# Kernel optimization log

Measured on AMD Instinct MI355X. Metric: run time of the kernel, lower is better.

## Reference

```python
import jax, jax.numpy as jnp
import numpy as np

NUM_HEADS = 4
KSIZE = 3
PAD = KSIZE // 2


def setup_inputs() -> dict:
    key = jax.random.key(0)
    ks = jax.random.split(key, 7)
    C = 128
    D = H = W = 24
    B = 1
    N = D * H * W
    std = 0.02
    return {
        "x": jax.random.normal(ks[0], (B, N, C), dtype=jnp.float32),
        "Wq": jax.random.normal(ks[1], (C, C), dtype=jnp.float32) * std,
        "bq": jnp.zeros((C,), dtype=jnp.float32),
        "Wkv": jax.random.normal(ks[2], (C, 2 * C), dtype=jnp.float32) * std,
        "bkv": jnp.zeros((2 * C,), dtype=jnp.float32),
        "Wp": jax.random.normal(ks[3], (C, C), dtype=jnp.float32) * std,
        "bp": jnp.zeros((C,), dtype=jnp.float32),
        "D": D,
        "H": H,
        "W": W,
    }


def reference(x, Wq, bq, Wkv, bkv, Wp, bp, D, H, W):
    B, N, C = x.shape
    nh = NUM_HEADS
    hc = C // nh
    scale = hc ** -0.5
    k = KSIZE
    K3 = k * k * k

    xv = x.reshape(B, D, H, W, C)
    # q: (B, D, H, W, nh, hc), pre-scaled
    q = (xv @ Wq + bq).reshape(B, D, H, W, nh, hc) * scale
    # kv: (B, D, H, W, 2, nh, hc)
    kv = (xv @ Wkv + bkv).reshape(B, D, H, W, 2, nh, hc)
    # zero-pad spatial dims (ZeroPad3d with pad_size = k//2)
    kvp = jnp.pad(kv, ((0, 0), (PAD, PAD), (PAD, PAD), (PAD, PAD), (0, 0), (0, 0), (0, 0)))
    # gather 3x3x3 neighborhoods via shifted slices (equivalent to unfold with stride=1)
    # nb: (B, D, H, W, K3, 2, nh, hc)
    nb = jnp.stack(
        [kvp[:, i:i + D, j:j + H, l:l + W]
         for i in range(k) for j in range(k) for l in range(k)],
        axis=4,
    )
    k_nb = nb[..., 0, :, :]  # (B,D,H,W,K3,nh,hc)
    v_nb = nb[..., 1, :, :]
    # per-voxel attention over K3 neighbors
    attn = jnp.einsum("bdhwnc,bdhwknc->bdhwnk", q, k_nb)
    attn = jax.nn.softmax(attn, axis=-1)
    out = jnp.einsum("bdhwnk,bdhwknc->bdhwnc", attn, v_nb)
    out = out.reshape(B, D, H, W, C) @ Wp + bp
    return out.reshape(B, N, C)
```

## Files before the change

### kernel.cpp

```cpp
#include <hip/hip_runtime.h>
#include <math.h>

#define NTOK 13824
#define CCH 128
#define DD3 24
#define SCALE 0.17677669529663687f
#define HSTRIDE 136

typedef float  f32x4  __attribute__((ext_vector_type(4)));
typedef short  s16x8  __attribute__((ext_vector_type(8)));

__device__ __forceinline__ ushort bf16_rtn(float f) {
    unsigned u = __float_as_uint(f);
    unsigned r = u + 0x7fffu + ((u >> 16) & 1u);
    return (ushort)(r >> 16);
}
__device__ __forceinline__ float bf16_f32(ushort h) {
    return __uint_as_float(((unsigned)h) << 16);
}

#define BSW(n, g) ((n) * 128 + ((((g) ^ ((n) & 7))) << 3))

__global__ __launch_bounds__(256) void prep_w(
    const float* __restrict__ Wq, const float* __restrict__ Wkv,
    const float* __restrict__ Wp, ushort* __restrict__ wimg)
{
    const int i   = blockIdx.x * 256 + threadIdx.x;
    const int seg = i >> 11;
    const int r   = i & 2047;
    const int n   = r & 63;
    const int k4  = (r >> 6) * 4;
    const float* W; int ldw, scol;
    if (seg < 2)      { W = Wq;  ldw = 128; scol = seg * 64; }
    else if (seg < 6) { W = Wkv; ldw = 256; scol = (seg - 2) * 64; }
    else              { W = Wp;  ldw = 128; scol = (seg - 6) * 64; }
    ushort4 hi, lo;
    float v;
    v = W[(k4 + 0) * ldw + scol + n]; hi.x = bf16_rtn(v); lo.x = bf16_rtn(v - bf16_f32(hi.x));
    v = W[(k4 + 1) * ldw + scol + n]; hi.y = bf16_rtn(v); lo.y = bf16_rtn(v - bf16_f32(hi.y));
    v = W[(k4 + 2) * ldw + scol + n]; hi.z = bf16_rtn(v); lo.z = bf16_rtn(v - bf16_f32(hi.z));
    v = W[(k4 + 3) * ldw + scol + n]; hi.w = bf16_rtn(v); lo.w = bf16_rtn(v - bf16_f32(hi.w));
    const int g = k4 >> 3;
    const int f = seg * 16384 + BSW(n, g) + (k4 & 7);
    *(ushort4*)(wimg + f)        = hi;
    *(ushort4*)(wimg + f + 8192) = lo;
}

__global__ __launch_bounds__(256) void qkv_fused(
    const float* __restrict__ x, const ushort* __restrict__ wimg,
    const float* __restrict__ bq, const float* __restrict__ bkv,
    float* __restrict__ qb, ushort* __restrict__ kvb)
{
    __shared__ ushort bsh[2][8192];

    const int t  = threadIdx.x;
    const int y  = blockIdx.y;
    const int wv = t >> 6, l = t & 63;

    const char* wseg = (const char*)(wimg + y * 16384);
    #pragma unroll
    for (int p = 0; p < 8; ++p) {
        const int chunk = (wv * 8 + p) * 1024;
        __builtin_amdgcn_global_load_lds(
            (const __attribute__((address_space(1))) void*)(wseg + chunk + l * 16),
            (__attribute__((address_space(3))) void*)((char*)bsh + chunk),
            16, 0, 0);
    }

    const int lm = l & 15, lk = l >> 4;
    const int row = blockIdx.x * 64 + wv * 16 + lm;
    const int ko  = lk * 8;

    s16x8 ah[4], al[4];
    #pragma unroll
    for (int kb = 0; kb < 4; ++kb) {
        const int k0 = kb * 32;
        const float4 a0 = *(const float4*)(x + row * 128 + k0 + ko);
        const float4 a1 = *(const float4*)(x + row * 128 + k0 + ko + 4);
        const float av[8] = {a0.x, a0.y, a0.z, a0.w, a1.x, a1.y, a1.z, a1.w};
        #pragma unroll
        for (int e = 0; e < 8; ++e) {
            const ushort hh = bf16_rtn(av[e]);
            ah[kb][e] = (short)hh;
            al[kb][e] = (short)bf16_rtn(av[e] - bf16_f32(hh));
        }
    }

    __syncthreads();

    f32x4 acc[4];
    #pragma unroll
    for (int nt = 0; nt < 4; ++nt)
        #pragma unroll
        for (int r = 0; r < 4; ++r) acc[nt][r] = 0.f;

    #pragma unroll
    for (int nt = 0; nt < 4; ++nt) {
        const int n = nt * 16 + lm;
        s16x8 bh[4], bl[4];
        #pragma unroll
        for (int kb = 0; kb < 4; ++kb) {
            const int g = kb * 4 + lk;
            bh[kb] = *(const s16x8*)(&bsh[0][BSW(n, g)]);
            bl[kb] = *(const s16x8*)(&bsh[1][BSW(n, g)]);
        }
        #pragma unroll
        for (int kb = 0; kb < 4; ++kb) {
            acc[nt] = __builtin_amdgcn_mfma_f32_16x16x32_bf16(ah[kb], bh[kb], acc[nt], 0, 0, 0);
            acc[nt] = __builtin_amdgcn_mfma_f32_16x16x32_bf16(ah[kb], bl[kb], acc[nt], 0, 0, 0);
            acc[nt] = __builtin_amdgcn_mfma_f32_16x16x32_bf16(al[kb], bh[kb], acc[nt], 0, 0, 0);
        }
    }

    const int orow0 = blockIdx.x * 64 + wv * 16 + lk * 4;
    #pragma unroll
    for (int nt = 0; nt < 4; ++nt) {
        const int col = y * 64 + nt * 16 + lm;
        if (col < 128) {
            const float b = bq[col];
            #pragma unroll
            for (int r = 0; r < 4; ++r)
                qb[(orow0 + r) * 128 + col] = (acc[nt][r] + b) * SCALE;
        } else {
            const int c2 = col - 128;
            const float b = bkv[c2];
            #pragma unroll
            for (int r = 0; r < 4; ++r)
                kvb[(orow0 + r) * 256 + c2] = bf16_rtn(acc[nt][r] + b);
        }
    }
}

__global__ __launch_bounds__(256) void attn3d(
    const float* __restrict__ qb, const ushort* __restrict__ kvb,
    ushort* __restrict__ aoh)
{
    __shared__ ushort sk[144 * HSTRIDE];

    const int t  = threadIdx.x;
    const int b  = blockIdx.x;
    const int tw = b % 6, th = (b / 6) % 6, td = b / 36;
    const int d0 = td * 2, h0 = th * 4, w0 = tw * 4;

    const int vox = t >> 3;
    const int q8  = t & 7;
    const int ld = vox >> 4, lh = (vox >> 2) & 3, lw = vox & 3;
    const int n  = ((d0 + ld) * DD3 + (h0 + lh)) * DD3 + (w0 + lw);
    const int choff = q8 * 16;

    float qv[16];
    #pragma unroll
    for (int m = 0; m < 4; ++m) {
        const float4 qq = *(const float4*)(qb + n * 128 + choff + m * 4);
        qv[m * 4 + 0] = qq.x; qv[m * 4 + 1] = qq.y;
        qv[m * 4 + 2] = qq.z; qv[m * 4 + 3] = qq.w;
    }

    #pragma unroll
    for (int p = 0; p < 9; ++p) {
        const int e = p * 256 + t;
        const int r = e >> 4;
        const int c = e & 15;
        const int a = r / 36, bb = (r / 6) % 6, cc = r % 6;
        const int gd = d0 - 1 + a, gh = h0 - 1 + bb, gw = w0 - 1 + cc;
        int4 v = {0, 0, 0, 0};
        if ((unsigned)gd < DD3 && (unsigned)gh < DD3 && (unsigned)gw < DD3) {
            const int n2 = (gd * DD3 + gh) * DD3 + gw;
            v = *(const int4*)(kvb + n2 * 256 + c * 8);
        }
        *(int4*)(sk + r * HSTRIDE + c * 8) = v;
    }
    __syncthreads();

    const int vbase = (ld * 36 + lh * 6 + lw);
    const ushort* kvoxel = sk + vbase * HSTRIDE + choff;

    float logit[27];
    #pragma unroll
    for (int i = 0; i < 3; ++i)
        #pragma unroll
        for (int j = 0; j < 3; ++j)
            #pragma unroll
            for (int l2 = 0; l2 < 3; ++l2) {
                const int idx = (i * 3 + j) * 3 + l2;
                const ushort* kr = kvoxel + (i * 36 + j * 6 + l2) * HSTRIDE;
                const int4 ka = *(const int4*)(kr);
                const int4 kb2 = *(const int4*)(kr + 8);
                float p = 0.f;
                const int* kwa = (const int*)&ka;
                const int* kwb = (const int*)&kb2;
                #pragma unroll
                for (int m = 0; m < 4; ++m) {
                    const unsigned u = (unsigned)kwa[m];
                    p = fmaf(qv[2 * m],     __uint_as_float(u << 16),        p);
                    p = fmaf(qv[2 * m + 1], __uint_as_float(u & 0xffff0000u), p);
                }
                #pragma unroll
                for (int m = 0; m < 4; ++m) {
                    const unsigned u = (unsigned)kwb[m];
                    p = fmaf(qv[8 + 2 * m],     __uint_as_float(u << 16),        p);
                    p = fmaf(qv[8 + 2 * m + 1], __uint_as_float(u & 0xffff0000u), p);
                }
                p += __shfl_xor(p, 1);
                logit[idx] = p;
            }

    float m0;
    {
        float t1[14];
        #pragma unroll
        for (int k = 0; k < 13; ++k) t1[k] = fmaxf(logit[2 * k], logit[2 * k + 1]);
        t1[13] = logit[26];
        float t2[7];
        #pragma unroll
        for (int k = 0; k < 7; ++k) t2[k] = fmaxf(t1[2 * k], t1[2 * k + 1]);
        m0 = fmaxf(fmaxf(fmaxf(t2[0], t2[1]), fmaxf(t2[2], t2[3])),
                   fmaxf(fmaxf(t2[4], t2[5]), t2[6]));
    }
    float s;
    {
        #pragma unroll
        for (int idx = 0; idx < 27; ++idx) logit[idx] = __expf(logit[idx] - m0);
        float t1[14];
        #pragma unroll
        for (int k = 0; k < 13; ++k) t1[k] = logit[2 * k] + logit[2 * k + 1];
        t1[13] = logit[26];
        float t2[7];
        #pragma unroll
        for (int k = 0; k < 7; ++k) t2[k] = t1[2 * k] + t1[2 * k + 1];
        s = ((t2[0] + t2[1]) + (t2[2] + t2[3])) + ((t2[4] + t2[5]) + t2[6]);
    }
    const float inv = 1.f / s;

    __syncthreads();

    #pragma unroll
    for (int p = 0; p < 9; ++p) {
        const int e = p * 256 + t;
        const int r = e >> 4;
        const int c = e & 15;
        const int a = r / 36, bb = (r / 6) % 6, cc = r % 6;
        const int gd = d0 - 1 + a, gh = h0 - 1 + bb, gw = w0 - 1 + cc;
        int4 v = {0, 0, 0, 0};
        if ((unsigned)gd < DD3 && (unsigned)gh < DD3 && (unsigned)gw < DD3) {
            const int n2 = (gd * DD3 + gh) * DD3 + gw;
            v = *(const int4*)(kvb + n2 * 256 + 128 + c * 8);
        }
        *(int4*)(sk + r * HSTRIDE + c * 8) = v;
    }
    __syncthreads();

    float acc[16];
    #pragma unroll
    for (int m = 0; m < 16; ++m) acc[m] = 0.f;

    #pragma unroll
    for (int i = 0; i < 3; ++i)
        #pragma unroll
        for (int j = 0; j < 3; ++j)
            #pragma unroll
            for (int l2 = 0; l2 < 3; ++l2) {
                const int idx = (i * 3 + j) * 3 + l2;
                const float p = logit[idx];
                const ushort* vr = kvoxel + (i * 36 + j * 6 + l2) * HSTRIDE;
                const int4 va = *(const int4*)(vr);
                const int4 vb2 = *(const int4*)(vr + 8);
                const int* vwa = (const int*)&va;
                const int* vwb = (const int*)&vb2;
                #pragma unroll
                for (int m = 0; m < 4; ++m) {
                    const unsigned u = (unsigned)vwa[m];
                    acc[2 * m]     = fmaf(p, __uint_as_float(u << 16),         acc[2 * m]);
                    acc[2 * m + 1] = fmaf(p, __uint_as_float(u & 0xffff0000u), acc[2 * m + 1]);
                }
                #pragma unroll
                for (int m = 0; m < 4; ++m) {
                    const unsigned u = (unsigned)vwb[m];
                    acc[8 + 2 * m]     = fmaf(p, __uint_as_float(u << 16),         acc[8 + 2 * m]);
                    acc[8 + 2 * m + 1] = fmaf(p, __uint_as_float(u & 0xffff0000u), acc[8 + 2 * m + 1]);
                }
            }

    int pk[8];
    #pragma unroll
    for (int m = 0; m < 8; ++m) {
        const float e0 = acc[2 * m] * inv;
        const float e1 = acc[2 * m + 1] * inv;
        pk[m] = (int)bf16_rtn(e0) | ((int)bf16_rtn(e1) << 16);
    }
    int4 o0 = {pk[0], pk[1], pk[2], pk[3]};
    int4 o1 = {pk[4], pk[5], pk[6], pk[7]};
    *(int4*)(aoh + n * 128 + choff)     = o0;
    *(int4*)(aoh + n * 128 + choff + 8) = o1;
}

__global__ __launch_bounds__(256) void proj_fused(
    const ushort* __restrict__ aoh, const ushort* __restrict__ wimg,
    const float* __restrict__ bp, float* __restrict__ out)
{
    __shared__ ushort bsh[2][8192];

    const int t  = threadIdx.x;
    const int wv = t >> 6, l = t & 63;

    const char* wseg = (const char*)(wimg + (6 + blockIdx.y) * 16384);
    #pragma unroll
    for (int p = 0; p < 8; ++p) {
        const int chunk = (wv * 8 + p) * 1024;
        __builtin_amdgcn_global_load_lds(
            (const __attribute__((address_space(1))) void*)(wseg + chunk + l * 16),
            (__attribute__((address_space(3))) void*)((char*)bsh + chunk),
            16, 0, 0);
    }

    const int lm = l & 15, lk = l >> 4;
    const int row = blockIdx.x * 64 + wv * 16 + lm;
    const int ko  = lk * 8;

    s16x8 ah[4];
    #pragma unroll
    for (int kb = 0; kb < 4; ++kb)
        ah[kb] = *(const s16x8*)(aoh + row * 128 + kb * 32 + ko);

    __syncthreads();

    f32x4 acc[4];
    #pragma unroll
    for (int nt = 0; nt < 4; ++nt)
        #pragma unroll
        for (int r = 0; r < 4; ++r) acc[nt][r] = 0.f;

    #pragma unroll
    for (int nt = 0; nt < 4; ++nt) {
        const int n = nt * 16 + lm;
        s16x8 bh[4], bl[4];
        #pragma unroll
        for (int kb = 0; kb < 4; ++kb) {
            const int g = kb * 4 + lk;
            bh[kb] = *(const s16x8*)(&bsh[0][BSW(n, g)]);
            bl[kb] = *(const s16x8*)(&bsh[1][BSW(n, g)]);
        }
        #pragma unroll
        for (int kb = 0; kb < 4; ++kb) {
            acc[nt] = __builtin_amdgcn_mfma_f32_16x16x32_bf16(ah[kb], bh[kb], acc[nt], 0, 0, 0);
            acc[nt] = __builtin_amdgcn_mfma_f32_16x16x32_bf16(ah[kb], bl[kb], acc[nt], 0, 0, 0);
        }
    }

    const int orow0 = blockIdx.x * 64 + wv * 16 + lk * 4;
    #pragma unroll
    for (int nt = 0; nt < 4; ++nt) {
        const int col = blockIdx.y * 64 + nt * 16 + lm;
        const float b = bp[col];
        #pragma unroll
        for (int r = 0; r < 4; ++r)
            out[(orow0 + r) * 128 + col] = acc[nt][r] + b;
    }
}

extern "C" void kernel_launch(void* const* d_in, const int* in_sizes, int n_in,
                              void* d_out, int out_size, void* d_ws, size_t ws_size,
                              hipStream_t stream) {
    const float* x   = (const float*)d_in[0];
    const float* Wq  = (const float*)d_in[1];
    const float* bq  = (const float*)d_in[2];
    const float* Wkv = (const float*)d_in[3];
    const float* bkv = (const float*)d_in[4];
    const float* Wp  = (const float*)d_in[5];
    const float* bp  = (const float*)d_in[6];
    float* out = (float*)d_out;

    char* ws = (char*)d_ws;
    float*  qb   = (float*)(ws);
    ushort* kvb  = (ushort*)(ws + 7077888);
    ushort* aoh  = (ushort*)(ws + 14155776);
    ushort* wimg = (ushort*)(ws + 17694720);

    prep_w<<<64, 256, 0, stream>>>(Wq, Wkv, Wp, wimg);
    dim3 g1(NTOK / 64, 6);
    qkv_fused<<<g1, 256, 0, stream>>>(x, wimg, bq, bkv, qb, kvb);
    attn3d<<<432, 256, 0, stream>>>(qb, kvb, aoh);
    dim3 g2(NTOK / 64, 2);
    proj_fused<<<g2, 256, 0, stream>>>(aoh, wimg, bp, out);
}
```

Before: 47.17 us.

## Fuse weight prep into QKV kernel and projection into attention kernel

Drops the separate weight-prep kernel: each QKV block now converts its own weight slice to split bf16 hi/lo directly into LDS, and a few blocks also prepare the Wp image. The attention kernel then performs the output projection itself, staging normalized attention outputs in LDS and running MFMA on them, which removes the intermediate attention-output buffer and two kernel launches. The cost is redundant weight conversion in every QKV block, larger LDS use in the attention kernel (lower occupancy), and a cross-kernel dependence on the Wp image written by the first kernel.

```diff
diff --git a/kernel.cpp b/kernel.cpp
--- a/kernel.cpp
+++ b/kernel.cpp
@@ -21,52 +21,58 @@
 
 #define BSW(n, g) ((n) * 128 + ((((g) ^ ((n) & 7))) << 3))
 
-__global__ __launch_bounds__(256) void prep_w(
-    const float* __restrict__ Wq, const float* __restrict__ Wkv,
-    const float* __restrict__ Wp, ushort* __restrict__ wimg)
-{
-    const int i   = blockIdx.x * 256 + threadIdx.x;
-    const int seg = i >> 11;
-    const int r   = i & 2047;
-    const int n   = r & 63;
-    const int k4  = (r >> 6) * 4;
-    const float* W; int ldw, scol;
-    if (seg < 2)      { W = Wq;  ldw = 128; scol = seg * 64; }
-    else if (seg < 6) { W = Wkv; ldw = 256; scol = (seg - 2) * 64; }
-    else              { W = Wp;  ldw = 128; scol = (seg - 6) * 64; }
-    ushort4 hi, lo;
-    float v;
-    v = W[(k4 + 0) * ldw + scol + n]; hi.x = bf16_rtn(v); lo.x = bf16_rtn(v - bf16_f32(hi.x));
-    v = W[(k4 + 1) * ldw + scol + n]; hi.y = bf16_rtn(v); lo.y = bf16_rtn(v - bf16_f32(hi.y));
-    v = W[(k4 + 2) * ldw + scol + n]; hi.z = bf16_rtn(v); lo.z = bf16_rtn(v - bf16_f32(hi.z));
-    v = W[(k4 + 3) * ldw + scol + n]; hi.w = bf16_rtn(v); lo.w = bf16_rtn(v - bf16_f32(hi.w));
-    const int g = k4 >> 3;
-    const int f = seg * 16384 + BSW(n, g) + (k4 & 7);
-    *(ushort4*)(wimg + f)        = hi;
-    *(ushort4*)(wimg + f + 8192) = lo;
-}
-
-__global__ __launch_bounds__(256) void qkv_fused(
-    const float* __restrict__ x, const ushort* __restrict__ wimg,
-    const float* __restrict__ bq, const float* __restrict__ bkv,
-    float* __restrict__ qb, ushort* __restrict__ kvb)
+__global__ __launch_bounds__(256) void qkv_all(
+    const float* __restrict__ x,
+    const float* __restrict__ Wq, const float* __restrict__ bq,
+    const float* __restrict__ Wkv, const float* __restrict__ bkv,
+    const float* __restrict__ Wp,
+    float* __restrict__ qb, ushort* __restrict__ kvb, ushort* __restrict__ wimg)
 {
     __shared__ ushort bsh[2][8192];
 
     const int t  = threadIdx.x;
     const int y  = blockIdx.y;
+
+    if (y == 5 && blockIdx.x < 16) {
+        const int i    = 12288 + blockIdx.x * 256 + t;
+        const int seg  = i >> 11;
+        const int r    = i & 2047;
+        const int n    = r & 63;
+        const int k4   = (r >> 6) * 4;
+        const int scol = (seg - 6) * 64;
+        ushort4 hi, lo;
+        float v;
+        v = Wp[(k4 + 0) * 128 + scol + n]; hi.x = bf16_rtn(v); lo.x = bf16_rtn(v - bf16_f32(hi.x));
+        v = Wp[(k4 + 1) * 128 + scol + n]; hi.y = bf16_rtn(v); lo.y = bf16_rtn(v - bf16_f32(hi.y));
+        v = Wp[(k4 + 2) * 128 + scol + n]; hi.z = bf16_rtn(v); lo.z = bf16_rtn(v - bf16_f32(hi.z));
+        v = Wp[(k4 + 3) * 128 + scol + n]; hi.w = bf16_rtn(v); lo.w = bf16_rtn(v - bf16_f32(hi.w));
+        const int f = seg * 16384 + BSW(n, k4 >> 3) + (k4 & 7);
+        *(ushort4*)(wimg + f)        = hi;
+        *(ushort4*)(wimg + f + 8192) = lo;
+    }
+
+    const float* W;
+    int ldw, scol;
+    if (y < 2) { W = Wq;  ldw = 128; scol = y * 64; }
+    else       { W = Wkv; ldw = 256; scol = (y - 2) * 64; }
+
+    #pragma unroll
+    for (int p = 0; p < 8; ++p) {
+        const int idx = p * 256 + t;
+        const int n   = idx & 63;
+        const int k4  = (idx >> 6) * 4;
+        ushort4 hi, lo;
+        float v;
+        v = W[(k4 + 0) * ldw + scol + n]; hi.x = bf16_rtn(v); lo.x = bf16_rtn(v - bf16_f32(hi.x));
+        v = W[(k4 + 1) * ldw + scol + n]; hi.y = bf16_rtn(v); lo.y = bf16_rtn(v - bf16_f32(hi.y));
+        v = W[(k4 + 2) * ldw + scol + n]; hi.z = bf16_rtn(v); lo.z = bf16_rtn(v - bf16_f32(hi.z));
+        v = W[(k4 + 3) * ldw + scol + n]; hi.w = bf16_rtn(v); lo.w = bf16_rtn(v - bf16_f32(hi.w));
+        const int e = BSW(n, k4 >> 3) + (k4 & 7);
+        *(ushort4*)(&bsh[0][e]) = hi;
+        *(ushort4*)(&bsh[1][e]) = lo;
+    }
+
     const int wv = t >> 6, l = t & 63;
-
-    const char* wseg = (const char*)(wimg + y * 16384);
-    #pragma unroll
-    for (int p = 0; p < 8; ++p) {
-        const int chunk = (wv * 8 + p) * 1024;
-        __builtin_amdgcn_global_load_lds(
-            (const __attribute__((address_space(1))) void*)(wseg + chunk + l * 16),
-            (__attribute__((address_space(3))) void*)((char*)bsh + chunk),
-            16, 0, 0);
-    }
-
     const int lm = l & 15, lk = l >> 4;
     const int row = blockIdx.x * 64 + wv * 16 + lm;
     const int ko  = lk * 8;
@@ -131,15 +137,19 @@
     }
 }
 
-__global__ __launch_bounds__(256) void attn3d(
+__global__ __launch_bounds__(256) void attn_proj(
     const float* __restrict__ qb, const ushort* __restrict__ kvb,
-    ushort* __restrict__ aoh)
+    const ushort* __restrict__ wimg, const float* __restrict__ bp,
+    float* __restrict__ out)
 {
-    __shared__ ushort sk[144 * HSTRIDE];
-
-    const int t  = threadIdx.x;
-    const int b  = blockIdx.x;
-    const int tw = b % 6, th = (b / 6) % 6, td = b / 36;
+    __shared__ ushort smem[36864];
+
+    const int t   = threadIdx.x;
+    const int bid = blockIdx.x;
+    const int wv = t >> 6, l = t & 63;
+    const int lm = l & 15, lk = l >> 4;
+
+    const int tw = bid % 6, th = (bid / 6) % 6, td = bid / 36;
     const int d0 = td * 2, h0 = th * 4, w0 = tw * 4;
 
     const int vox = t >> 3;
@@ -168,12 +178,12 @@
             const int n2 = (gd * DD3 + gh) * DD3 + gw;
             v = *(const int4*)(kvb + n2 * 256 + c * 8);
         }
-        *(int4*)(sk + r * HSTRIDE + c * 8) = v;
+        *(int4*)(smem + r * HSTRIDE + c * 8) = v;
     }
     __syncthreads();
 
     const int vbase = (ld * 36 + lh * 6 + lw);
-    const ushort* kvoxel = sk + vbase * HSTRIDE + choff;
+    const ushort* kvoxel = smem + vbase * HSTRIDE + choff;
 
     float logit[27];
     #pragma unroll
@@ -192,13 +202,13 @@
                 #pragma unroll
                 for (int m = 0; m < 4; ++m) {
                     const unsigned u = (unsigned)kwa[m];
-                    p = fmaf(qv[2 * m],     __uint_as_float(u << 16),        p);
+                    p = fmaf(qv[2 * m],     __uint_as_float(u << 16),         p);
                     p = fmaf(qv[2 * m + 1], __uint_as_float(u & 0xffff0000u), p);
                 }
                 #pragma unroll
                 for (int m = 0; m < 4; ++m) {
                     const unsigned u = (unsigned)kwb[m];
-                    p = fmaf(qv[8 + 2 * m],     __uint_as_float(u << 16),        p);
+                    p = fmaf(qv[8 + 2 * m],     __uint_as_float(u << 16),         p);
                     p = fmaf(qv[8 + 2 * m + 1], __uint_as_float(u & 0xffff0000u), p);
                 }
                 p += __shfl_xor(p, 1);
@@ -217,7 +227,7 @@
         m0 = fmaxf(fmaxf(fmaxf(t2[0], t2[1]), fmaxf(t2[2], t2[3])),
                    fmaxf(fmaxf(t2[4], t2[5]), t2[6]));
     }
-    float s;
+    float sden;
     {
         #pragma unroll
         for (int idx = 0; idx < 27; ++idx) logit[idx] = __expf(logit[idx] - m0);
@@ -228,9 +238,9 @@
         float t2[7];
         #pragma unroll
         for (int k = 0; k < 7; ++k) t2[k] = t1[2 * k] + t1[2 * k + 1];
-        s = ((t2[0] + t2[1]) + (t2[2] + t2[3])) + ((t2[4] + t2[5]) + t2[6]);
-    }
-    const float inv = 1.f / s;
+        sden = ((t2[0] + t2[1]) + (t2[2] + t2[3])) + ((t2[4] + t2[5]) + t2[6]);
+    }
+    const float inv = 1.f / sden;
 
     __syncthreads();
 
@@ -246,7 +256,7 @@
             const int n2 = (gd * DD3 + gh) * DD3 + gw;
             v = *(const int4*)(kvb + n2 * 256 + 128 + c * 8);
         }
-        *(int4*)(sk + r * HSTRIDE + c * 8) = v;
+        *(int4*)(smem + r * HSTRIDE + c * 8) = v;
     }
     __syncthreads();
 
@@ -281,81 +291,87 @@
                 }
             }
 
-    int pk[8];
-    #pragma unroll
-    for (int m = 0; m < 8; ++m) {
-        const float e0 = acc[2 * m] * inv;
-        const float e1 = acc[2 * m + 1] * inv;
-        pk[m] = (int)bf16_rtn(e0) | ((int)bf16_rtn(e1) << 16);
-    }
-    int4 o0 = {pk[0], pk[1], pk[2], pk[3]};
-    int4 o1 = {pk[4], pk[5], pk[6], pk[7]};
-    *(int4*)(aoh + n * 128 + choff)     = o0;
-    *(int4*)(aoh + n * 128 + choff + 8) = o1;
-}
-
-__global__ __launch_bounds__(256) void proj_fused(
-    const ushort* __restrict__ aoh, const ushort* __restrict__ wimg,
-    const float* __restrict__ bp, float* __restrict__ out)
-{
-    __shared__ ushort bsh[2][8192];
-
-    const int t  = threadIdx.x;
-    const int wv = t >> 6, l = t & 63;
-
-    const char* wseg = (const char*)(wimg + (6 + blockIdx.y) * 16384);
-    #pragma unroll
-    for (int p = 0; p < 8; ++p) {
-        const int chunk = (wv * 8 + p) * 1024;
+    __syncthreads();
+
+    const char* wsrc = (const char*)(wimg + 6 * 16384);
+    #pragma unroll
+    for (int p = 0; p < 16; ++p) {
+        const int chunk = (wv * 16 + p) * 1024;
         __builtin_amdgcn_global_load_lds(
-            (const __attribute__((address_space(1))) void*)(wseg + chunk + l * 16),
-            (__attribute__((address_space(3))) void*)((char*)bsh + chunk),
+            (const __attribute__((address_space(1))) void*)(wsrc + chunk + l * 16),
+            (__attribute__((address_space(3))) void*)((char*)smem + chunk),
             16, 0, 0);
     }
 
-    const int lm = l & 15, lk = l >> 4;
-    const int row = blockIdx.x * 64 + wv * 16 + lm;
-    const int ko  = lk * 8;
-
-    s16x8 ah[4];
-    #pragma unroll
-    for (int kb = 0; kb < 4; ++kb)
-        ah[kb] = *(const s16x8*)(aoh + row * 128 + kb * 32 + ko);
-
-    __syncthreads();
-
-    f32x4 acc[4];
-    #pragma unroll
-    for (int nt = 0; nt < 4; ++nt)
-        #pragma unroll
-        for (int r = 0; r < 4; ++r) acc[nt][r] = 0.f;
-
-    #pragma unroll
-    for (int nt = 0; nt < 4; ++nt) {
-        const int n = nt * 16 + lm;
+    {
+        ushort hv[16];
+        #pragma unroll
+        for (int m = 0; m < 16; ++m) hv[m] = bf16_rtn(acc[m] * inv);
+        const int g0 = q8 * 2;
+        const int e0 = vox * 128 + (((g0)     ^ (vox & 7)) << 3);
+        const int e1 = vox * 128 + (((g0 + 1) ^ (vox & 7)) << 3);
+        ushort4 w0 = {hv[0], hv[1], hv[2], hv[3]};
+        ushort4 w1 = {hv[4], hv[5], hv[6], hv[7]};
+        ushort4 w2 = {hv[8], hv[9], hv[10], hv[11]};
+        ushort4 w3 = {hv[12], hv[13], hv[14], hv[15]};
+        *(ushort4*)(smem + 32768 + e0)     = w0;
+        *(ushort4*)(smem + 32768 + e0 + 4) = w1;
+        *(ushort4*)(smem + 32768 + e1)     = w2;
+        *(ushort4*)(smem + 32768 + e1 + 4) = w3;
+    }
+    __syncthreads();
+
+    s16x8 pa[2][4];
+    #pragma unroll
+    for (int rt2 = 0; rt2 < 2; ++rt2)
+        #pragma unroll
+        for (int kb = 0; kb < 4; ++kb)
+            pa[rt2][kb] = *(const s16x8*)(smem + 32768 + BSW(rt2 * 16 + lm, kb * 4 + lk));
+
+    const int ncol = wv * 32;
+    f32x4 acc2[2][2];
+    #pragma unroll
+    for (int rt2 = 0; rt2 < 2; ++rt2)
+        #pragma unroll
+        for (int ct = 0; ct < 2; ++ct)
+            #pragma unroll
+            for (int r = 0; r < 4; ++r) acc2[rt2][ct][r] = 0.f;
+
+    #pragma unroll
+    for (int ct = 0; ct < 2; ++ct) {
+        const int nc = ncol + ct * 16 + lm;
+        const int hb = (nc >= 64) ? 16384 : 0;
+        const int nn = nc & 63;
         s16x8 bh[4], bl[4];
         #pragma unroll
         for (int kb = 0; kb < 4; ++kb) {
             const int g = kb * 4 + lk;
-            bh[kb] = *(const s16x8*)(&bsh[0][BSW(n, g)]);
-            bl[kb] = *(const s16x8*)(&bsh[1][BSW(n, g)]);
-        }
-        #pragma unroll
-        for (int kb = 0; kb < 4; ++kb) {
-            acc[nt] = __builtin_amdgcn_mfma_f32_16x16x32_bf16(ah[kb], bh[kb], acc[nt], 0, 0, 0);
-            acc[nt] = __builtin_amdgcn_mfma_f32_16x16x32_bf16(ah[kb], bl[kb], acc[nt], 0, 0, 0);
-        }
-    }
-
-    const int orow0 = blockIdx.x * 64 + wv * 16 + lk * 4;
-    #pragma unroll
-    for (int nt = 0; nt < 4; ++nt) {
-        const int col = blockIdx.y * 64 + nt * 16 + lm;
-        const float b = bp[col];
-        #pragma unroll
-        for (int r = 0; r < 4; ++r)
-            out[(orow0 + r) * 128 + col] = acc[nt][r] + b;
-    }
+            bh[kb] = *(const s16x8*)(smem + hb + BSW(nn, g));
+            bl[kb] = *(const s16x8*)(smem + hb + 8192 + BSW(nn, g));
+        }
+        #pragma unroll
+        for (int rt2 = 0; rt2 < 2; ++rt2)
+            #pragma unroll
+            for (int kb = 0; kb < 4; ++kb) {
+                acc2[rt2][ct] = __builtin_amdgcn_mfma_f32_16x16x32_bf16(pa[rt2][kb], bh[kb], acc2[rt2][ct], 0, 0, 0);
+                acc2[rt2][ct] = __builtin_amdgcn_mfma_f32_16x16x32_bf16(pa[rt2][kb], bl[kb], acc2[rt2][ct], 0, 0, 0);
+            }
+    }
+
+    #pragma unroll
+    for (int rt2 = 0; rt2 < 2; ++rt2)
+        #pragma unroll
+        for (int ct = 0; ct < 2; ++ct) {
+            const int col = ncol + ct * 16 + lm;
+            const float bb = bp[col];
+            #pragma unroll
+            for (int r = 0; r < 4; ++r) {
+                const int vox3 = rt2 * 16 + lk * 4 + r;
+                const int ld3 = vox3 >> 4, lh3 = (vox3 >> 2) & 3, lw3 = vox3 & 3;
+                const int n3 = ((d0 + ld3) * DD3 + (h0 + lh3)) * DD3 + (w0 + lw3);
+                out[n3 * 128 + col] = acc2[rt2][ct][r] + bb;
+            }
+        }
 }
 
 extern "C" void kernel_launch(void* const* d_in, const int* in_sizes, int n_in,
@@ -373,13 +389,9 @@
     char* ws = (char*)d_ws;
     float*  qb   = (float*)(ws);
     ushort* kvb  = (ushort*)(ws + 7077888);
-    ushort* aoh  = (ushort*)(ws + 14155776);
-    ushort* wimg = (ushort*)(ws + 17694720);
-
-    prep_w<<<64, 256, 0, stream>>>(Wq, Wkv, Wp, wimg);
+    ushort* wimg = (ushort*)(ws + 14155776);
+
     dim3 g1(NTOK / 64, 6);
-    qkv_fused<<<g1, 256, 0, stream>>>(x, wimg, bq, bkv, qb, kvb);
-    attn3d<<<432, 256, 0, stream>>>(qb, kvb, aoh);
-    dim3 g2(NTOK / 64, 2);
-    proj_fused<<<g2, 256, 0, stream>>>(aoh, wimg, bp, out);
-}
+    qkv_all<<<g1, 256, 0, stream>>>(x, Wq, bq, Wkv, bkv, Wp, qb, kvb, wimg);
+    attn_proj<<<432, 256, 0, stream>>>(qb, kvb, wimg, bp, out);
+}
```

After: 39.75 us. -15.7%, faster.
